# Kernel tuning notes

Hardware: AMD Instinct MI355X
Metric: run time of the kernel (lower is better)

## Reference

```python
import jax, jax.numpy as jnp
import numpy as np

B, S, D, H = 4, 2048, 1024, 16
DH = D // H


def setup_inputs() -> dict:
    key = jax.random.key(0)
    k1, k2, k3, k4, k5 = jax.random.split(key, 5)
    X = jax.random.normal(k1, (B, S, D), dtype=jnp.float32)
    W1 = jax.random.normal(k2, (3 * D, D), dtype=jnp.float32) * 0.02
    b1 = jax.random.normal(k3, (3 * D,), dtype=jnp.float32) * 0.01
    W2 = jax.random.normal(k4, (D, D), dtype=jnp.float32) * 0.02
    b2 = jax.random.normal(k5, (D,), dtype=jnp.float32) * 0.01
    return {"X": X, "W1": W1, "b1": b1, "W2": W2, "b2": b2}


def reference(X, W1, b1, W2, b2):
    b, s, d = X.shape
    # fused QKV projection (nn.Linear: y = x @ W.T + b)
    Y = X @ W1.T + b1                                   # [B,S,3D]
    Q, K, V = jnp.split(Y, 3, axis=2)                   # each [B,S,D]
    # reshape(x): view (B,S,H,DH) then permute(0,2,3,1) -> [B,H,DH,S]
    q = Q.reshape(b, s, H, DH).transpose(0, 2, 3, 1)    # [B,H,DH,S]
    v = V.reshape(b, s, H, DH).transpose(0, 2, 3, 1)    # [B,H,DH,S]
    # reshape(x, k=True): permute(0,2,1,3) -> [B,H,S,DH]
    k = K.reshape(b, s, H, DH).transpose(0, 2, 1, 3)    # [B,H,S,DH]
    # w = q @ k / sqrt(q.size(-1)) ; note q.size(-1) == S in this layout
    w = jnp.einsum('bhds,bhse->bhde', q, k) / jnp.sqrt(jnp.asarray(s, X.dtype))  # [B,H,DH,DH]
    w = jax.nn.softmax(w, axis=-1)
    out = jnp.einsum('bhde,bhes->bhds', w, v)           # [B,H,DH,S]
    # cat(): raw contiguous view of [B,H,DH,S] into [B,S,H*DH] (memory-order reshape)
    out = out.reshape(b, s, H * DH)                     # [B,S,D]
    return out @ W2.T + b2
```

## Files before the change

kernel.cpp:

```cpp
#include <hip/hip_runtime.h>
#include <stdint.h>

#define B_ 4
#define S_ 2048
#define D_ 1024
#define H_ 16
#define DH_ 64
#define M_TOT (B_*S_)
#define N1_ (3*D_)
#define K_ D_
#define NCH 8

typedef __bf16 bf16_8 __attribute__((ext_vector_type(8)));
typedef float  f32x4  __attribute__((ext_vector_type(4)));

typedef __attribute__((address_space(1))) const void* gas_t;
typedef __attribute__((address_space(3))) void*       las_t;

__device__ __forceinline__ unsigned short f2bf(float f) {
    union { float f; unsigned u; } v; v.f = f;
    unsigned r = v.u + 0x7FFFu + ((v.u >> 16) & 1u);
    return (unsigned short)(r >> 16);
}

__device__ __forceinline__ void async_ld16(const void* g, void* l) {
    __builtin_amdgcn_global_load_lds((gas_t)g, (las_t)l, 16, 0, 0);
}

__global__ __launch_bounds__(256)
void cast_kernel(const float* __restrict__ X, const float* __restrict__ W1,
                 const float* __restrict__ W2, unsigned short* __restrict__ Xb,
                 unsigned short* __restrict__ W1b, unsigned short* __restrict__ W2b) {
    const int nX  = (M_TOT * K_) / 4;
    const int nW1 = (N1_ * K_) / 4;
    int i = blockIdx.x * 256 + threadIdx.x;
    const float4* src; unsigned short* dst; int j;
    if (i < nX)            { src = (const float4*)X;  dst = Xb;  j = i; }
    else if (i < nX + nW1) { src = (const float4*)W1; dst = W1b; j = i - nX; }
    else                   { src = (const float4*)W2; dst = W2b; j = i - nX - nW1; }
    float4 v = src[j];
    ushort4 o;
    o.x = f2bf(v.x); o.y = f2bf(v.y); o.z = f2bf(v.z); o.w = f2bf(v.w);
    ((ushort4*)dst)[j] = o;
}

template<int N, bool OUT_BF16>
__global__ __launch_bounds__(256)
void gemm_bt(const unsigned short* __restrict__ A,
             const unsigned short* __restrict__ Bm,
             const float* __restrict__ bias,
             void* __restrict__ C, int K) {
    __shared__ unsigned short As[128 * 32];
    __shared__ unsigned short Bs[128 * 32];
    const int t    = threadIdx.x;
    const int wid  = t >> 6;
    const int lane = t & 63;
    const int lrow = lane & 15;
    const int lq   = lane >> 4;
    const int m0   = blockIdx.y * 128;
    const int n0   = blockIdx.x * 128;
    const int wm   = (wid >> 1) * 64;
    const int wn   = (wid & 1) * 64;

    f32x4 acc[4][4] = {};

    const int c0 = t, c1 = t + 256;
    const int r0 = c0 >> 2, kc0 = (c0 & 3) * 8;
    const int r1 = c1 >> 2, kc1 = (c1 & 3) * 8;

    for (int k0 = 0; k0 < K; k0 += 32) {
        async_ld16(A  + (size_t)(m0 + r0) * K + k0 + kc0, (char*)As + c0 * 16);
        async_ld16(A  + (size_t)(m0 + r1) * K + k0 + kc1, (char*)As + c1 * 16);
        async_ld16(Bm + (size_t)(n0 + r0) * K + k0 + kc0, (char*)Bs + c0 * 16);
        async_ld16(Bm + (size_t)(n0 + r1) * K + k0 + kc1, (char*)Bs + c1 * 16);
        __syncthreads();

        const unsigned short* ap = As + (wm + lrow) * 32 + lq * 8;
        const unsigned short* bp = Bs + (wn + lrow) * 32 + lq * 8;
        bf16_8 af[4], bfr[4];
#pragma unroll
        for (int mt = 0; mt < 4; mt++) af[mt]  = *(const bf16_8*)(ap + mt * 512);
#pragma unroll
        for (int nt = 0; nt < 4; nt++) bfr[nt] = *(const bf16_8*)(bp + nt * 512);
#pragma unroll
        for (int mt = 0; mt < 4; mt++)
#pragma unroll
            for (int nt = 0; nt < 4; nt++)
                acc[mt][nt] = __builtin_amdgcn_mfma_f32_16x16x32_bf16(af[mt], bfr[nt], acc[mt][nt], 0, 0, 0);
        __syncthreads();
    }

#pragma unroll
    for (int nt = 0; nt < 4; nt++) {
        const int col = n0 + wn + nt * 16 + lrow;
        const float bv = bias[col];
#pragma unroll
        for (int mt = 0; mt < 4; mt++) {
            const int row = m0 + wm + mt * 16 + lq * 4;
            f32x4 a = acc[mt][nt];
            if (OUT_BF16) {
                unsigned short* Cp = (unsigned short*)C;
#pragma unroll
                for (int i = 0; i < 4; i++)
                    Cp[(size_t)(row + i) * N + col] = f2bf(a[i] + bv);
            } else {
                float* Cp = (float*)C;
#pragma unroll
                for (int i = 0; i < 4; i++)
                    Cp[(size_t)(row + i) * N + col] = a[i] + bv;
            }
        }
    }
}

__global__ __launch_bounds__(256)
void attn_scores(const unsigned short* __restrict__ Y, float* __restrict__ Scp) {
    __shared__ unsigned short Qs[64 * 72];
    __shared__ unsigned short Ks[64 * 72];
    const int bh = blockIdx.x, ch = blockIdx.y;
    const int b = bh >> 4, h = bh & 15;
    const size_t ybase = (size_t)b * S_ * 3072;
    const int qoff = h * 64, koff = D_ + h * 64;
    const int t = threadIdx.x, wid = t >> 6, lane = t & 63;
    const int lrow = lane & 15, lq = lane >> 4;

    f32x4 acc[4] = {};
    const int sbeg = ch * (S_ / NCH);
    for (int s0 = sbeg; s0 < sbeg + S_ / NCH; s0 += 64) {
#pragma unroll
        for (int p = 0; p < 4; p++) {
            int idx = p * 256 + t;
            int r = idx >> 4, cg = (idx & 15) * 4;
            const size_t gb = ybase + (size_t)(s0 + r) * 3072;
            ushort4 q4 = *(const ushort4*)(Y + gb + qoff + cg);
            ushort4 k4 = *(const ushort4*)(Y + gb + koff + cg);
            Qs[(cg + 0) * 72 + r] = q4.x; Qs[(cg + 1) * 72 + r] = q4.y;
            Qs[(cg + 2) * 72 + r] = q4.z; Qs[(cg + 3) * 72 + r] = q4.w;
            Ks[(cg + 0) * 72 + r] = k4.x; Ks[(cg + 1) * 72 + r] = k4.y;
            Ks[(cg + 2) * 72 + r] = k4.z; Ks[(cg + 3) * 72 + r] = k4.w;
        }
        __syncthreads();
#pragma unroll
        for (int ks = 0; ks < 2; ks++) {
            bf16_8 aq = *(const bf16_8*)(Qs + (wid * 16 + lrow) * 72 + ks * 32 + lq * 8);
#pragma unroll
            for (int nt = 0; nt < 4; nt++) {
                bf16_8 bk = *(const bf16_8*)(Ks + (nt * 16 + lrow) * 72 + ks * 32 + lq * 8);
                acc[nt] = __builtin_amdgcn_mfma_f32_16x16x32_bf16(aq, bk, acc[nt], 0, 0, 0);
            }
        }
        __syncthreads();
    }

    float* out = Scp + (size_t)(bh * NCH + ch) * 64 * 64;
#pragma unroll
    for (int nt = 0; nt < 4; nt++)
#pragma unroll
        for (int i = 0; i < 4; i++)
            out[(wid * 16 + lq * 4 + i) * 64 + nt * 16 + lrow] = acc[nt][i];
}

__global__ __launch_bounds__(256)
void attn_softmax(const float* __restrict__ Scp, unsigned short* __restrict__ Wb) {
    const int bh = blockIdx.x;
    const int t = threadIdx.x;
    const int d = t >> 2, q = t & 3;
    float s[16] = {};
#pragma unroll
    for (int c = 0; c < NCH; c++) {
        const float4* p = (const float4*)(Scp + ((size_t)(bh * NCH + c) * 64 + d) * 64 + q * 16);
#pragma unroll
        for (int j = 0; j < 4; j++) {
            float4 v = p[j];
            s[j*4+0] += v.x; s[j*4+1] += v.y; s[j*4+2] += v.z; s[j*4+3] += v.w;
        }
    }
    const float scale = 0.022097086912079608f;
    float m = -3.0e38f;
#pragma unroll
    for (int i = 0; i < 16; i++) { s[i] *= scale; m = fmaxf(m, s[i]); }
    m = fmaxf(m, __shfl_xor(m, 1));
    m = fmaxf(m, __shfl_xor(m, 2));
    float sum = 0.f;
#pragma unroll
    for (int i = 0; i < 16; i++) { s[i] = __expf(s[i] - m); sum += s[i]; }
    sum += __shfl_xor(sum, 1);
    sum += __shfl_xor(sum, 2);
    const float inv = 1.0f / sum;
    unsigned short* w = Wb + (size_t)bh * 4096 + d * 64 + q * 16;
    ushort4 o0, o1, o2, o3;
    o0.x=f2bf(s[0]*inv);  o0.y=f2bf(s[1]*inv);  o0.z=f2bf(s[2]*inv);  o0.w=f2bf(s[3]*inv);
    o1.x=f2bf(s[4]*inv);  o1.y=f2bf(s[5]*inv);  o1.z=f2bf(s[6]*inv);  o1.w=f2bf(s[7]*inv);
    o2.x=f2bf(s[8]*inv);  o2.y=f2bf(s[9]*inv);  o2.z=f2bf(s[10]*inv); o2.w=f2bf(s[11]*inv);
    o3.x=f2bf(s[12]*inv); o3.y=f2bf(s[13]*inv); o3.z=f2bf(s[14]*inv); o3.w=f2bf(s[15]*inv);
    ((ushort4*)w)[0]=o0; ((ushort4*)w)[1]=o1; ((ushort4*)w)[2]=o2; ((ushort4*)w)[3]=o3;
}

__global__ __launch_bounds__(256)
void attn_out(const unsigned short* __restrict__ Y, const unsigned short* __restrict__ Wb,
              unsigned short* __restrict__ O) {
    __shared__ unsigned short Ws[64 * 72];
    const int bh = blockIdx.x, sc = blockIdx.y;
    const int b = bh >> 4, h = bh & 15;
    const size_t ybase = (size_t)b * S_ * 3072;
    const int voff = 2 * D_ + h * 64;
    const int t = threadIdx.x, wid = t >> 6, lane = t & 63;
    const int lrow = lane & 15, lq = lane >> 4;

    {
        const int d = t >> 2, q = t & 3;
        const uint4* src = (const uint4*)(Wb + (size_t)bh * 4096 + d * 64 + q * 16);
        uint4* dst = (uint4*)(Ws + d * 72 + q * 16);
        dst[0] = src[0];
        *(uint4*)(Ws + d * 72 + q * 16 + 8) = src[1];
    }
    __syncthreads();

    bf16_8 aw[4][2];
#pragma unroll
    for (int mt = 0; mt < 4; mt++)
#pragma unroll
        for (int ks = 0; ks < 2; ks++)
            aw[mt][ks] = *(const bf16_8*)(Ws + (mt * 16 + lrow) * 72 + ks * 32 + lq * 8);

    const size_t obase = (size_t)b * (H_ * DH_ * S_) + (size_t)h * (DH_ * S_);
    const int s0 = sc * 256 + wid * 64;
    f32x4 o[4][4] = {};
#pragma unroll
    for (int ks = 0; ks < 2; ks++) {
        bf16_8 bv[4];
#pragma unroll
        for (int nt = 0; nt < 4; nt++)
            bv[nt] = *(const bf16_8*)(Y + ybase + (size_t)(s0 + nt * 16 + lrow) * 3072 + voff + ks * 32 + lq * 8);
#pragma unroll
        for (int mt = 0; mt < 4; mt++)
#pragma unroll
            for (int nt = 0; nt < 4; nt++)
                o[mt][nt] = __builtin_amdgcn_mfma_f32_16x16x32_bf16(aw[mt][ks], bv[nt], o[mt][nt], 0, 0, 0);
    }
#pragma unroll
    for (int mt = 0; mt < 4; mt++)
#pragma unroll
        for (int nt = 0; nt < 4; nt++) {
            const int d = mt * 16 + lq * 4;
            const int s = s0 + nt * 16 + lrow;
#pragma unroll
            for (int i = 0; i < 4; i++)
                O[obase + (size_t)(d + i) * S_ + s] = f2bf(o[mt][nt][i]);
        }
}

extern "C" void kernel_launch(void* const* d_in, const int* in_sizes, int n_in,
                              void* d_out, int out_size, void* d_ws, size_t ws_size,
                              hipStream_t stream) {
    const float* X  = (const float*)d_in[0];
    const float* W1 = (const float*)d_in[1];
    const float* b1 = (const float*)d_in[2];
    const float* W2 = (const float*)d_in[3];
    const float* b2 = (const float*)d_in[4];

    char* ws = (char*)d_ws;
    unsigned short* Xb  = (unsigned short*)(ws + 0);
    unsigned short* W1b = (unsigned short*)(ws + (16u << 20));
    unsigned short* W2b = (unsigned short*)(ws + (22u << 20));
    unsigned short* Yb  = (unsigned short*)(ws + (24u << 20));
    unsigned short* Wb  = (unsigned short*)(ws + 0);
    unsigned short* Ob  = (unsigned short*)(ws + (1u << 20));
    float* Scp = (float*)d_out;

    cast_kernel<<<12288, 256, 0, stream>>>(X, W1, W2, Xb, W1b, W2b);
    gemm_bt<N1_, true><<<dim3(N1_ / 128, M_TOT / 128), 256, 0, stream>>>(Xb, W1b, b1, Yb, K_);
    attn_scores<<<dim3(64, NCH), 256, 0, stream>>>(Yb, Scp);
    attn_softmax<<<64, 256, 0, stream>>>(Scp, Wb);
    attn_out<<<dim3(64, NCH), 256, 0, stream>>>(Yb, Wb, Ob);
    gemm_bt<D_, false><<<dim3(D_ / 128, M_TOT / 128), 256, 0, stream>>>(Ob, W2b, b2, d_out, K_);
}
```

Baseline: 237.7 us.

## Double GEMM K-tile to 64 and XOR-swizzle LDS layout

The GEMM main loop now stages a 64-wide K slab per iteration instead of 32, halving the number of barrier pairs per K sweep. The LDS layout is XOR-swizzled by row so that fragment reads across the 16 rows of a lane group land in different banks. This is meant to cut barrier overhead and LDS bank conflicts, at the cost of doubling shared memory per block, which may reduce occupancy.

```diff
diff --git a/kernel.cpp b/kernel.cpp
--- a/kernel.cpp
+++ b/kernel.cpp
@@ -50,8 +50,8 @@
              const unsigned short* __restrict__ Bm,
              const float* __restrict__ bias,
              void* __restrict__ C, int K) {
-    __shared__ unsigned short As[128 * 32];
-    __shared__ unsigned short Bs[128 * 32];
+    __shared__ unsigned short As[128 * 64];
+    __shared__ unsigned short Bs[128 * 64];
     const int t    = threadIdx.x;
     const int wid  = t >> 6;
     const int lane = t & 63;
@@ -64,29 +64,38 @@
 
     f32x4 acc[4][4] = {};
 
-    const int c0 = t, c1 = t + 256;
-    const int r0 = c0 >> 2, kc0 = (c0 & 3) * 8;
-    const int r1 = c1 >> 2, kc1 = (c1 & 3) * 8;
-
-    for (int k0 = 0; k0 < K; k0 += 32) {
-        async_ld16(A  + (size_t)(m0 + r0) * K + k0 + kc0, (char*)As + c0 * 16);
-        async_ld16(A  + (size_t)(m0 + r1) * K + k0 + kc1, (char*)As + c1 * 16);
-        async_ld16(Bm + (size_t)(n0 + r0) * K + k0 + kc0, (char*)Bs + c0 * 16);
-        async_ld16(Bm + (size_t)(n0 + r1) * K + k0 + kc1, (char*)Bs + c1 * 16);
-        __syncthreads();
-
-        const unsigned short* ap = As + (wm + lrow) * 32 + lq * 8;
-        const unsigned short* bp = Bs + (wn + lrow) * 32 + lq * 8;
-        bf16_8 af[4], bfr[4];
-#pragma unroll
-        for (int mt = 0; mt < 4; mt++) af[mt]  = *(const bf16_8*)(ap + mt * 512);
-#pragma unroll
-        for (int nt = 0; nt < 4; nt++) bfr[nt] = *(const bf16_8*)(bp + nt * 512);
-#pragma unroll
-        for (int mt = 0; mt < 4; mt++)
-#pragma unroll
-            for (int nt = 0; nt < 4; nt++)
-                acc[mt][nt] = __builtin_amdgcn_mfma_f32_16x16x32_bf16(af[mt], bfr[nt], acc[mt][nt], 0, 0, 0);
+    for (int k0 = 0; k0 < K; k0 += 64) {
+#pragma unroll
+        for (int p = 0; p < 4; p++) {
+            const int c   = p * 256 + t;
+            const int row = c >> 3;
+            const int kb  = (c & 7) ^ (row & 7);
+            async_ld16(A  + (size_t)(m0 + row) * K + k0 + kb * 8, (char*)As + c * 16);
+            async_ld16(Bm + (size_t)(n0 + row) * K + k0 + kb * 8, (char*)Bs + c * 16);
+        }
+        __syncthreads();
+
+#pragma unroll
+        for (int ks = 0; ks < 2; ks++) {
+            bf16_8 af[4], bfr[4];
+#pragma unroll
+            for (int mt = 0; mt < 4; mt++) {
+                const int r  = wm + mt * 16 + lrow;
+                const int kb = (ks * 4 + lq) ^ (r & 7);
+                af[mt] = *(const bf16_8*)(As + (r * 8 + kb) * 8);
+            }
+#pragma unroll
+            for (int nt = 0; nt < 4; nt++) {
+                const int r  = wn + nt * 16 + lrow;
+                const int kb = (ks * 4 + lq) ^ (r & 7);
+                bfr[nt] = *(const bf16_8*)(Bs + (r * 8 + kb) * 8);
+            }
+#pragma unroll
+            for (int mt = 0; mt < 4; mt++)
+#pragma unroll
+                for (int nt = 0; nt < 4; nt++)
+                    acc[mt][nt] = __builtin_amdgcn_mfma_f32_16x16x32_bf16(af[mt], bfr[nt], acc[mt][nt], 0, 0, 0);
+        }
         __syncthreads();
     }
 
```

Result: faster. 212.3 us (-10.7%).
